# Performance work log

Measured on AMD Instinct MI355X. Metric: run time of the kernel, lower is better.

The kernel has to match this reference:

```python
import jax, jax.numpy as jnp
import numpy as np

B, S, D_IN, D_OUT = 4, 2048, 1024, 1024


def setup_inputs() -> dict:
    key = jax.random.key(0)
    ks = jax.random.split(key, 7)
    s_in = 1.0 / np.sqrt(D_IN)
    return {
        "x": jax.random.normal(ks[0], (B, S, D_IN), dtype=jnp.float32),
        "Wq": jax.random.uniform(ks[1], (D_IN, D_OUT), jnp.float32, -s_in, s_in),
        "bq": jax.random.uniform(ks[2], (D_OUT,), jnp.float32, -s_in, s_in),
        "Wk": jax.random.uniform(ks[3], (D_IN, D_OUT), jnp.float32, -s_in, s_in),
        "bk": jax.random.uniform(ks[4], (D_OUT,), jnp.float32, -s_in, s_in),
        "Wv": jax.random.uniform(ks[5], (D_IN, D_OUT), jnp.float32, -s_in, s_in),
        "bv": jax.random.uniform(ks[6], (D_OUT,), jnp.float32, -s_in, s_in),
    }


def reference(x, Wq, bq, Wk, bk, Wv, bv):
    # q,k,v: [B, S, D_OUT]
    q = jnp.einsum("bsd,de->bse", x, Wq) + bq
    k = jnp.einsum("bsd,de->bse", x, Wk) + bk
    v = jnp.einsum("bsd,de->bse", x, Wv) + bv
    scale = 1.0 / jnp.sqrt(jnp.asarray(q.shape[-1], q.dtype))
    scores = jnp.einsum("bqe,bke->bqk", q, k) * scale  # [B, S, S]
    attn = jax.nn.softmax(scores, axis=-1)
    return jnp.einsum("bqk,bke->bqe", attn, v)
```

## Files before the change

kernel.cpp:

```cpp
#include <hip/hip_runtime.h>
#include <hip/hip_bf16.h>
#include <stdint.h>


#define Bsz 4
#define Ssz 2048
#define Dsz 1024

typedef __attribute__((ext_vector_type(8))) short short8;
typedef __attribute__((ext_vector_type(4))) float floatx4;
typedef const __attribute__((address_space(1))) void* gptr_t;
typedef __attribute__((address_space(3))) void* lptr_t;

__device__ __forceinline__ ushort f32_to_bf16(float f) {
    union { float f; uint32_t u; } c; c.f = f;
    uint32_t u = c.u;
    u += 0x7fffu + ((u >> 16) & 1u);
    return (ushort)(u >> 16);
}

__global__ __launch_bounds__(256, 2) void k_qkv(
    const ushort* __restrict__ xb, const ushort* __restrict__ Wt,
    const float* __restrict__ bq, const float* __restrict__ bk,
    const float* __restrict__ bv, ushort* __restrict__ QKV,
    ushort* __restrict__ Vt)
{
    __shared__ ushort lsA[2][128 * 32];
    __shared__ ushort lsB[2][3][128 * 32];

    const int tid  = threadIdx.x;
    const int bx   = blockIdx.x;
    const int by   = blockIdx.y;
    const int row0 = by * 128;
    const int col0 = bx * 128;

    const int lane = tid & 63;
    const int wave = tid >> 6;
    const int wr   = (wave >> 1) * 64;
    const int wc   = (wave & 1) * 64;
    const int m16  = lane & 15;
    const int quad = lane >> 4;

    floatx4 acc[3][4][4];
#pragma unroll
    for (int z = 0; z < 3; z++)
#pragma unroll
        for (int i = 0; i < 4; i++)
#pragma unroll
            for (int j = 0; j < 4; j++) acc[z][i][j] = (floatx4){0.f, 0.f, 0.f, 0.f};

    const int srow = tid >> 2;
    const int skc  = (tid & 3) ^ ((srow >> 1) & 3);
    const ushort* ga = xb + (size_t)(row0 + srow) * Dsz + skc * 8;
    const ushort* gb0 = Wt + (size_t)(col0 + srow) * Dsz + skc * 8;

    const int aoff = (quad ^ ((m16 >> 1) & 3)) * 8;

    __builtin_amdgcn_global_load_lds((gptr_t)(ga),                    (lptr_t)(lsA[0] + tid * 8),        16, 0, 0);
    __builtin_amdgcn_global_load_lds((gptr_t)(ga + (size_t)64 * Dsz), (lptr_t)(lsA[0] + 2048 + tid * 8), 16, 0, 0);
#pragma unroll
    for (int z = 0; z < 3; z++) {
        const ushort* gb = gb0 + (size_t)z * Dsz * Dsz;
        __builtin_amdgcn_global_load_lds((gptr_t)(gb),                    (lptr_t)(lsB[0][z] + tid * 8),        16, 0, 0);
        __builtin_amdgcn_global_load_lds((gptr_t)(gb + (size_t)64 * Dsz), (lptr_t)(lsB[0][z] + 2048 + tid * 8), 16, 0, 0);
    }

    for (int k0 = 0; k0 < Dsz; k0 += 32) {
        const int cur = (k0 >> 5) & 1;
        __syncthreads();
        if (k0 + 32 < Dsz) {
            const int nxt = cur ^ 1;
            const int kn = k0 + 32;
            __builtin_amdgcn_global_load_lds((gptr_t)(ga + kn),                    (lptr_t)(lsA[nxt] + tid * 8),        16, 0, 0);
            __builtin_amdgcn_global_load_lds((gptr_t)(ga + kn + (size_t)64 * Dsz), (lptr_t)(lsA[nxt] + 2048 + tid * 8), 16, 0, 0);
#pragma unroll
            for (int z = 0; z < 3; z++) {
                const ushort* gb = gb0 + (size_t)z * Dsz * Dsz + kn;
                __builtin_amdgcn_global_load_lds((gptr_t)(gb),                    (lptr_t)(lsB[nxt][z] + tid * 8),        16, 0, 0);
                __builtin_amdgcn_global_load_lds((gptr_t)(gb + (size_t)64 * Dsz), (lptr_t)(lsB[nxt][z] + 2048 + tid * 8), 16, 0, 0);
            }
        }

        short8 af[4];
#pragma unroll
        for (int mi = 0; mi < 4; mi++)
            af[mi] = *(const short8*)&lsA[cur][(wr + mi * 16 + m16) * 32 + aoff];
#pragma unroll
        for (int z = 0; z < 3; z++) {
            short8 bfr[4];
#pragma unroll
            for (int ni = 0; ni < 4; ni++)
                bfr[ni] = *(const short8*)&lsB[cur][z][(wc + ni * 16 + m16) * 32 + aoff];
#pragma unroll
            for (int mi = 0; mi < 4; mi++)
#pragma unroll
                for (int ni = 0; ni < 4; ni++)
                    acc[z][mi][ni] = __builtin_amdgcn_mfma_f32_16x16x32_bf16(af[mi], bfr[ni], acc[z][mi][ni], 0, 0, 0);
        }
    }

#pragma unroll
    for (int ni = 0; ni < 4; ni++) {
        const int gcol = col0 + wc + ni * 16 + m16;
        const float bqv = bq[gcol], bkv = bk[gcol], bvv = bv[gcol];
#pragma unroll
        for (int mi = 0; mi < 4; mi++) {
            const int grow0 = row0 + wr + mi * 16 + quad * 4;
            ushort4 vpack;
#pragma unroll
            for (int j = 0; j < 4; j++) {
                QKV[(size_t)(grow0 + j) * Dsz + gcol] = f32_to_bf16((acc[0][mi][ni][j] + bqv) * 0.03125f);
                QKV[(size_t)(Bsz * Ssz) * Dsz + (size_t)(grow0 + j) * Dsz + gcol] = f32_to_bf16(acc[1][mi][ni][j] + bkv);
                const ushort vv = f32_to_bf16(acc[2][mi][ni][j] + bvv);
                if (j == 0) vpack.x = vv; else if (j == 1) vpack.y = vv;
                else if (j == 2) vpack.z = vv; else vpack.w = vv;
            }
            const int batch = grow0 >> 11;
            const int s0 = grow0 & (Ssz - 1);
            *(ushort4*)&Vt[(size_t)batch * Dsz * Ssz + (size_t)gcol * Ssz + s0] = vpack;
        }
    }
}

__global__ __launch_bounds__(512, 2) void k_scores(
    const ushort* __restrict__ QKV, ushort* __restrict__ P,
    float* __restrict__ partial)
{
    __shared__ ushort lsA[2][256 * 32];
    __shared__ ushort lsB[2][256 * 32];
    __shared__ float  red[4][256];

    const int bid = blockIdx.x;
    const int bn  = bid & 7;
    const int i   = bid >> 3;
    const int bm  = i & 7;
    const int b   = i >> 3;
    const int row0 = bm * 256;
    const int col0 = bn * 256;

    const ushort* A  = QKV + (size_t)b * Ssz * Dsz;
    const ushort* Bt = QKV + (size_t)(Bsz + b) * Ssz * Dsz;
    ushort* Pb = P + (size_t)b * Ssz * Ssz;

    const int tid  = threadIdx.x;
    const int lane = tid & 63;
    const int wave = tid >> 6;
    const int wr   = (wave >> 2) * 128;
    const int wc   = (wave & 3) * 64;
    const int m16  = lane & 15;
    const int quad = lane >> 4;

    floatx4 acc[8][4];
#pragma unroll
    for (int mi = 0; mi < 8; mi++)
#pragma unroll
        for (int ni = 0; ni < 4; ni++) acc[mi][ni] = (floatx4){0.f, 0.f, 0.f, 0.f};

    const int srow = tid >> 2;
    const int skc  = (tid & 3) ^ ((srow >> 1) & 3);
    const ushort* ga = A  + (size_t)(row0 + srow) * Dsz + skc * 8;
    const ushort* gb = Bt + (size_t)(col0 + srow) * Dsz + skc * 8;
    const int aoff = (quad ^ ((m16 >> 1) & 3)) * 8;

    __builtin_amdgcn_global_load_lds((gptr_t)(ga),                      (lptr_t)(lsA[0] + tid * 8),        16, 0, 0);
    __builtin_amdgcn_global_load_lds((gptr_t)(ga + (size_t)128 * Dsz),  (lptr_t)(lsA[0] + 4096 + tid * 8), 16, 0, 0);
    __builtin_amdgcn_global_load_lds((gptr_t)(gb),                      (lptr_t)(lsB[0] + tid * 8),        16, 0, 0);
    __builtin_amdgcn_global_load_lds((gptr_t)(gb + (size_t)128 * Dsz),  (lptr_t)(lsB[0] + 4096 + tid * 8), 16, 0, 0);

    for (int k0 = 0; k0 < Dsz; k0 += 32) {
        const int cur = (k0 >> 5) & 1;
        __syncthreads();
        if (k0 + 32 < Dsz) {
            const int nxt = cur ^ 1;
            const int kn = k0 + 32;
            __builtin_amdgcn_global_load_lds((gptr_t)(ga + kn),                      (lptr_t)(lsA[nxt] + tid * 8),        16, 0, 0);
            __builtin_amdgcn_global_load_lds((gptr_t)(ga + kn + (size_t)128 * Dsz),  (lptr_t)(lsA[nxt] + 4096 + tid * 8), 16, 0, 0);
            __builtin_amdgcn_global_load_lds((gptr_t)(gb + kn),                      (lptr_t)(lsB[nxt] + tid * 8),        16, 0, 0);
            __builtin_amdgcn_global_load_lds((gptr_t)(gb + kn + (size_t)128 * Dsz),  (lptr_t)(lsB[nxt] + 4096 + tid * 8), 16, 0, 0);
        }

        short8 af[8], bfr[4];
#pragma unroll
        for (int mi = 0; mi < 8; mi++)
            af[mi] = *(const short8*)&lsA[cur][(wr + mi * 16 + m16) * 32 + aoff];
#pragma unroll
        for (int ni = 0; ni < 4; ni++)
            bfr[ni] = *(const short8*)&lsB[cur][(wc + ni * 16 + m16) * 32 + aoff];
#pragma unroll
        for (int mi = 0; mi < 8; mi++)
#pragma unroll
            for (int ni = 0; ni < 4; ni++)
                acc[mi][ni] = __builtin_amdgcn_mfma_f32_16x16x32_bf16(af[mi], bfr[ni], acc[mi][ni], 0, 0, 0);
    }

    float rs[8][4];
#pragma unroll
    for (int mi = 0; mi < 8; mi++)
#pragma unroll
        for (int j = 0; j < 4; j++) rs[mi][j] = 0.f;
#pragma unroll
    for (int ni = 0; ni < 4; ni++) {
        const int gcol = col0 + wc + ni * 16 + m16;
#pragma unroll
        for (int mi = 0; mi < 8; mi++) {
            const int grow0 = row0 + wr + mi * 16 + quad * 4;
#pragma unroll
            for (int j = 0; j < 4; j++) {
                const float e = __expf(acc[mi][ni][j]);
                Pb[(size_t)(grow0 + j) * Ssz + gcol] = f32_to_bf16(e);
                rs[mi][j] += e;
            }
        }
    }
#pragma unroll
    for (int mi = 0; mi < 8; mi++)
#pragma unroll
        for (int j = 0; j < 4; j++) {
            float v = rs[mi][j];
            v += __shfl_xor(v, 1, 64);
            v += __shfl_xor(v, 2, 64);
            v += __shfl_xor(v, 4, 64);
            v += __shfl_xor(v, 8, 64);
            if (m16 == 0) red[wave & 3][wr + mi * 16 + quad * 4 + j] = v;
        }
    __syncthreads();
    if (tid < 256) {
        const float s = red[0][tid] + red[1][tid] + red[2][tid] + red[3][tid];
        partial[(((size_t)b * 8 + bm) * 8 + bn) * 256 + tid] = s;
    }
}

__global__ __launch_bounds__(512, 1) void k_pv(
    const ushort* __restrict__ P, const ushort* __restrict__ Vt,
    const float* __restrict__ partial, float* __restrict__ out)
{
    __shared__ ushort lsA[2][128 * 32];
    __shared__ ushort lsB[2][256 * 32];
    __shared__ float  invs[128];

    const int bid = blockIdx.x;
    const int c   = bid & 7;
    const int i   = bid >> 3;
    const int bx  = i & 3;
    const int sid = c * 8 + (i >> 2);
    const int by  = sid & 15;
    const int b   = sid >> 4;
    const int row0 = by * 128;
    const int col0 = bx * 256;

    const ushort* A  = P  + (size_t)b * Ssz * Ssz;
    const ushort* Bt = Vt + (size_t)b * Dsz * Ssz;
    float* Cout = out + (size_t)b * Ssz * Dsz;
    const float* pin = partial + (size_t)b * 8 * 8 * 256;

    const int tid  = threadIdx.x;
    const int lane = tid & 63;
    const int wave = tid >> 6;
    const int wr   = (wave >> 2) * 64;
    const int wc   = (wave & 3) * 64;
    const int m16  = lane & 15;
    const int quad = lane >> 4;

    floatx4 acc[4][4];
#pragma unroll
    for (int i2 = 0; i2 < 4; i2++)
#pragma unroll
        for (int j = 0; j < 4; j++) acc[i2][j] = (floatx4){0.f, 0.f, 0.f, 0.f};

    if (tid < 128) {
        const int r = row0 + tid;
        const float* pb = pin + ((size_t)(r >> 8) * 8) * 256 + (r & 255);
        float s = 0.f;
#pragma unroll
        for (int bn = 0; bn < 8; bn++) s += pb[bn * 256];
        invs[tid] = 1.0f / s;
    }

    const int srow = tid >> 2;
    const int skc  = (tid & 3) ^ ((srow >> 1) & 3);
    const ushort* ga = A  + (size_t)(row0 + srow) * Ssz + skc * 8;
    const ushort* gb = Bt + (size_t)(col0 + srow) * Ssz + skc * 8;
    const int aoff = (quad ^ ((m16 >> 1) & 3)) * 8;

    __builtin_amdgcn_global_load_lds((gptr_t)(ga),                      (lptr_t)(lsA[0] + tid * 8),        16, 0, 0);
    __builtin_amdgcn_global_load_lds((gptr_t)(gb),                      (lptr_t)(lsB[0] + tid * 8),        16, 0, 0);
    __builtin_amdgcn_global_load_lds((gptr_t)(gb + (size_t)128 * Ssz),  (lptr_t)(lsB[0] + 4096 + tid * 8), 16, 0, 0);

    for (int k0 = 0; k0 < Ssz; k0 += 32) {
        const int cur = (k0 >> 5) & 1;
        __syncthreads();
        if (k0 + 32 < Ssz) {
            const int nxt = cur ^ 1;
            const int kn = k0 + 32;
            __builtin_amdgcn_global_load_lds((gptr_t)(ga + kn),                      (lptr_t)(lsA[nxt] + tid * 8),        16, 0, 0);
            __builtin_amdgcn_global_load_lds((gptr_t)(gb + kn),                      (lptr_t)(lsB[nxt] + tid * 8),        16, 0, 0);
            __builtin_amdgcn_global_load_lds((gptr_t)(gb + kn + (size_t)128 * Ssz),  (lptr_t)(lsB[nxt] + 4096 + tid * 8), 16, 0, 0);
        }

        short8 af[4], bfr[4];
#pragma unroll
        for (int mi = 0; mi < 4; mi++)
            af[mi] = *(const short8*)&lsA[cur][(wr + mi * 16 + m16) * 32 + aoff];
#pragma unroll
        for (int ni = 0; ni < 4; ni++)
            bfr[ni] = *(const short8*)&lsB[cur][(wc + ni * 16 + m16) * 32 + aoff];
#pragma unroll
        for (int mi = 0; mi < 4; mi++)
#pragma unroll
            for (int ni = 0; ni < 4; ni++)
                acc[mi][ni] = __builtin_amdgcn_mfma_f32_16x16x32_bf16(af[mi], bfr[ni], acc[mi][ni], 0, 0, 0);
    }

#pragma unroll
    for (int ni = 0; ni < 4; ni++) {
        const int gcol = col0 + wc + ni * 16 + m16;
#pragma unroll
        for (int mi = 0; mi < 4; mi++) {
            const int grow0 = row0 + wr + mi * 16 + quad * 4;
            const int rl0   = wr + mi * 16 + quad * 4;
#pragma unroll
            for (int j = 0; j < 4; j++)
                Cout[(size_t)(grow0 + j) * Dsz + gcol] = acc[mi][ni][j] * invs[rl0 + j];
        }
    }
}

__global__ __launch_bounds__(256) void k_prep(
    const float* __restrict__ x, ushort* __restrict__ xb,
    const float* __restrict__ Wq, const float* __restrict__ Wk,
    const float* __restrict__ Wv, ushort* __restrict__ Wt)
{
    __shared__ float tile[32][33];
    const int bid = blockIdx.x;
    const int tid = threadIdx.x;
    if (bid < 8192) {
        int i = (bid * 256 + tid) * 4;
        float4 v = *(const float4*)(x + i);
        ushort4 o;
        o.x = f32_to_bf16(v.x); o.y = f32_to_bf16(v.y);
        o.z = f32_to_bf16(v.z); o.w = f32_to_bf16(v.w);
        *(ushort4*)(xb + i) = o;
    } else {
        const int wb = bid - 8192;
        const int z  = wb >> 10;
        const int r  = wb & 1023;
        const int nb = (r & 31) * 32;
        const int kb = (r >> 5) * 32;
        const float* W = (z == 0) ? Wq : ((z == 1) ? Wk : Wv);
        ushort* out = Wt + (size_t)z * Dsz * Dsz;
        const int tx = tid & 31, ty = tid >> 5;
#pragma unroll
        for (int j = 0; j < 32; j += 8)
            tile[ty + j][tx] = W[(size_t)(kb + ty + j) * Dsz + nb + tx];
        __syncthreads();
#pragma unroll
        for (int j = 0; j < 32; j += 8)
            out[(size_t)(nb + ty + j) * Dsz + kb + tx] = f32_to_bf16(tile[tx][ty + j]);
    }
}

extern "C" void kernel_launch(void* const* d_in, const int* in_sizes, int n_in,
                              void* d_out, int out_size, void* d_ws, size_t ws_size,
                              hipStream_t stream) {
    const float* x  = (const float*)d_in[0];
    const float* Wq = (const float*)d_in[1];
    const float* bq = (const float*)d_in[2];
    const float* Wk = (const float*)d_in[3];
    const float* bk = (const float*)d_in[4];
    const float* Wv = (const float*)d_in[5];
    const float* bv = (const float*)d_in[6];
    float* out = (float*)d_out;

    char* ws = (char*)d_ws;
    ushort* xb      = (ushort*)(ws);
    ushort* Wt      = (ushort*)(ws + 16777216);
    ushort* QKV     = (ushort*)(ws + 23068672);
    ushort* Vt      = (ushort*)(ws + 73400320);
    ushort* P       = (ushort*)(ws + 90177536);
    float*  partial = (float*) (ws + 123731968);

    k_prep<<<dim3(8192 + 3072), dim3(256), 0, stream>>>(x, xb, Wq, Wk, Wv, Wt);
    k_qkv<<<dim3(Dsz / 128, Bsz * Ssz / 128), dim3(256), 0, stream>>>(xb, Wt, bq, bk, bv, QKV, Vt);
    k_scores<<<dim3(256), dim3(512), 0, stream>>>(QKV, P, partial);
    k_pv<<<dim3(256), dim3(512), 0, stream>>>(P, Vt, partial, out);
}
```

Before: 265.6 us.

## Restructure QK^T scores GEMM into fine-grained 8-phase pipelined schedule with K=64 tiles

```diff
diff --git a/kernel.cpp b/kernel.cpp
--- a/kernel.cpp
+++ b/kernel.cpp
@@ -17,6 +17,16 @@
     uint32_t u = c.u;
     u += 0x7fffu + ((u >> 16) & 1u);
     return (ushort)(u >> 16);
+}
+
+__device__ __forceinline__ void glds16(const ushort* g, ushort* l) {
+    __builtin_amdgcn_global_load_lds((gptr_t)g, (lptr_t)l, 16, 0, 0);
+}
+
+__device__ __forceinline__ void barrier_raw() {
+    asm volatile("" ::: "memory");
+    __builtin_amdgcn_s_barrier();
+    asm volatile("" ::: "memory");
 }
 
 __global__ __launch_bounds__(256, 2) void k_qkv(
@@ -122,33 +132,61 @@
     }
 }
 
+#define RD_A(QM, PAR)                                                          \
+    _Pragma("unroll") for (int mi_ = 0; mi_ < 4; mi_++) {                      \
+        const ushort* rp_ = &lsA[(PAR) * 2 + waveM][((QM) * 64 + mi_ * 16 + m16) * 64]; \
+        a0[mi_] = *(const short8*)(rp_ + csw);                                 \
+        a1[mi_] = *(const short8*)(rp_ + (csw ^ 32));                          \
+    }
+#define RD_B(QN, PAR, SET)                                                     \
+    _Pragma("unroll") for (int nj_ = 0; nj_ < 2; nj_++) {                      \
+        const ushort* rp_ = &lsB[(PAR) * 2 + bReg][(bRow0 + (QN) * 32 + nj_ * 16 + m16) * 64]; \
+        bb[SET][nj_][0] = *(const short8*)(rp_ + csw);                         \
+        bb[SET][nj_][1] = *(const short8*)(rp_ + (csw ^ 32));                  \
+    }
+#define MM(MH, NH, SET)                                                        \
+    _Pragma("unroll") for (int mi_ = 0; mi_ < 4; mi_++)                        \
+    _Pragma("unroll") for (int nj_ = 0; nj_ < 2; nj_++) {                      \
+        acc[(MH) * 4 + mi_][(NH) * 2 + nj_] = __builtin_amdgcn_mfma_f32_16x16x32_bf16( \
+            a0[mi_], bb[SET][nj_][0], acc[(MH) * 4 + mi_][(NH) * 2 + nj_], 0, 0, 0);   \
+        acc[(MH) * 4 + mi_][(NH) * 2 + nj_] = __builtin_amdgcn_mfma_f32_16x16x32_bf16( \
+            a1[mi_], bb[SET][nj_][1], acc[(MH) * 4 + mi_][(NH) * 2 + nj_], 0, 0, 0);   \
+    }
+
 __global__ __launch_bounds__(512, 2) void k_scores(
     const ushort* __restrict__ QKV, ushort* __restrict__ P,
     float* __restrict__ partial)
 {
-    __shared__ ushort lsA[2][256 * 32];
-    __shared__ ushort lsB[2][256 * 32];
-    __shared__ float  red[4][256];
+    __shared__ __align__(16) ushort lsA[4][8192];
+    __shared__ __align__(16) ushort lsB[4][8192];
+    __shared__ float red[4][256];
 
     const int bid = blockIdx.x;
     const int bn  = bid & 7;
-    const int i   = bid >> 3;
-    const int bm  = i & 7;
-    const int b   = i >> 3;
-    const int row0 = bm * 256;
-    const int col0 = bn * 256;
-
-    const ushort* A  = QKV + (size_t)b * Ssz * Dsz;
-    const ushort* Bt = QKV + (size_t)(Bsz + b) * Ssz * Dsz;
+    const int ii  = bid >> 3;
+    const int bm  = ii & 7;
+    const int b   = ii >> 3;
+    const int row0 = bm * 256, col0 = bn * 256;
+
+    const ushort* Aq = QKV + (size_t)b * Ssz * Dsz;
+    const ushort* Bk = QKV + (size_t)(Bsz + b) * Ssz * Dsz;
     ushort* Pb = P + (size_t)b * Ssz * Ssz;
 
-    const int tid  = threadIdx.x;
-    const int lane = tid & 63;
-    const int wave = tid >> 6;
-    const int wr   = (wave >> 2) * 128;
-    const int wc   = (wave & 3) * 64;
-    const int m16  = lane & 15;
-    const int quad = lane >> 4;
+    const int tid   = threadIdx.x;
+    const int lane  = tid & 63;
+    const int wave  = tid >> 6;
+    const int m16   = lane & 15;
+    const int quad  = lane >> 4;
+    const int waveM = wave >> 2;
+    const int waveN = wave & 3;
+    const int wr    = waveM * 128;
+    const int wc    = waveN * 64;
+    const int bReg  = waveN >> 1;
+    const int bRow0 = (waveN & 1) * 64;
+    const int csw   = (quad ^ (m16 & 7)) * 8;
+
+    const int sRow = tid >> 3;
+    const int sCol = ((tid & 7) ^ (sRow & 7)) * 8;
 
     floatx4 acc[8][4];
 #pragma unroll
@@ -156,41 +194,79 @@
 #pragma unroll
         for (int ni = 0; ni < 4; ni++) acc[mi][ni] = (floatx4){0.f, 0.f, 0.f, 0.f};
 
-    const int srow = tid >> 2;
-    const int skc  = (tid & 3) ^ ((srow >> 1) & 3);
-    const ushort* ga = A  + (size_t)(row0 + srow) * Dsz + skc * 8;
-    const ushort* gb = Bt + (size_t)(col0 + srow) * Dsz + skc * 8;
-    const int aoff = (quad ^ ((m16 >> 1) & 3)) * 8;
-
-    __builtin_amdgcn_global_load_lds((gptr_t)(ga),                      (lptr_t)(lsA[0] + tid * 8),        16, 0, 0);
-    __builtin_amdgcn_global_load_lds((gptr_t)(ga + (size_t)128 * Dsz),  (lptr_t)(lsA[0] + 4096 + tid * 8), 16, 0, 0);
-    __builtin_amdgcn_global_load_lds((gptr_t)(gb),                      (lptr_t)(lsB[0] + tid * 8),        16, 0, 0);
-    __builtin_amdgcn_global_load_lds((gptr_t)(gb + (size_t)128 * Dsz),  (lptr_t)(lsB[0] + 4096 + tid * 8), 16, 0, 0);
-
-    for (int k0 = 0; k0 < Dsz; k0 += 32) {
-        const int cur = (k0 >> 5) & 1;
-        __syncthreads();
-        if (k0 + 32 < Dsz) {
-            const int nxt = cur ^ 1;
-            const int kn = k0 + 32;
-            __builtin_amdgcn_global_load_lds((gptr_t)(ga + kn),                      (lptr_t)(lsA[nxt] + tid * 8),        16, 0, 0);
-            __builtin_amdgcn_global_load_lds((gptr_t)(ga + kn + (size_t)128 * Dsz),  (lptr_t)(lsA[nxt] + 4096 + tid * 8), 16, 0, 0);
-            __builtin_amdgcn_global_load_lds((gptr_t)(gb + kn),                      (lptr_t)(lsB[nxt] + tid * 8),        16, 0, 0);
-            __builtin_amdgcn_global_load_lds((gptr_t)(gb + kn + (size_t)128 * Dsz),  (lptr_t)(lsB[nxt] + 4096 + tid * 8), 16, 0, 0);
-        }
-
-        short8 af[8], bfr[4];
-#pragma unroll
-        for (int mi = 0; mi < 8; mi++)
-            af[mi] = *(const short8*)&lsA[cur][(wr + mi * 16 + m16) * 32 + aoff];
-#pragma unroll
-        for (int ni = 0; ni < 4; ni++)
-            bfr[ni] = *(const short8*)&lsB[cur][(wc + ni * 16 + m16) * 32 + aoff];
-#pragma unroll
-        for (int mi = 0; mi < 8; mi++)
-#pragma unroll
-            for (int ni = 0; ni < 4; ni++)
-                acc[mi][ni] = __builtin_amdgcn_mfma_f32_16x16x32_bf16(af[mi], bfr[ni], acc[mi][ni], 0, 0, 0);
+    auto stA = [&](int t, int half) {
+        ushort* d = &lsA[(t & 1) * 2 + half][0] + tid * 8;
+        const ushort* s = Aq + (size_t)(row0 + half * 128 + sRow) * Dsz + t * 64 + sCol;
+        glds16(s, d);
+        glds16(s + (size_t)64 * Dsz, d + 4096);
+    };
+    auto stB = [&](int t, int half) {
+        ushort* d = &lsB[(t & 1) * 2 + half][0] + tid * 8;
+        const ushort* s = Bk + (size_t)(col0 + half * 128 + sRow) * Dsz + t * 64 + sCol;
+        glds16(s, d);
+        glds16(s + (size_t)64 * Dsz, d + 4096);
+    };
+
+    short8 a0[4], a1[4], bb[2][2][2];
+
+    stB(0, 0); stB(0, 1);
+    stA(0, 0); stA(0, 1);
+    stB(1, 0); stB(1, 1);
+    asm volatile("s_waitcnt vmcnt(4)" ::: "memory");
+    barrier_raw();
+
+    for (int it = 0; it < 8; ++it) {
+        const int t0 = 2 * it, t1 = t0 + 1;
+        const bool s2 = (t0 + 2 < 16), s3 = (t1 + 2 < 16);
+
+        RD_A(0, 0); RD_B(0, 0, 0);
+        stA(t1, 0);
+        barrier_raw();
+        __builtin_amdgcn_s_setprio(1); MM(0, 0, 0); __builtin_amdgcn_s_setprio(0);
+        barrier_raw();
+
+        RD_B(1, 0, 1);
+        stA(t1, 1);
+        barrier_raw();
+        __builtin_amdgcn_s_setprio(1); MM(0, 1, 1); __builtin_amdgcn_s_setprio(0);
+        barrier_raw();
+
+        RD_A(1, 0);
+        if (s2) stB(t0 + 2, 0);
+        barrier_raw();
+        __builtin_amdgcn_s_setprio(1); MM(1, 1, 1); __builtin_amdgcn_s_setprio(0);
+        barrier_raw();
+
+        if (s2) stB(t0 + 2, 1);
+        barrier_raw();
+        __builtin_amdgcn_s_setprio(1); MM(1, 0, 0); __builtin_amdgcn_s_setprio(0);
+        if (s2) { asm volatile("s_waitcnt vmcnt(4)" ::: "memory"); }
+        else    { asm volatile("s_waitcnt vmcnt(0)" ::: "memory"); }
+        barrier_raw();
+
+        RD_A(0, 1); RD_B(0, 1, 0);
+        if (s2) stA(t0 + 2, 0);
+        barrier_raw();
+        __builtin_amdgcn_s_setprio(1); MM(0, 0, 0); __builtin_amdgcn_s_setprio(0);
+        barrier_raw();
+
+        RD_B(1, 1, 1);
+        if (s2) stA(t0 + 2, 1);
+        barrier_raw();
+        __builtin_amdgcn_s_setprio(1); MM(0, 1, 1); __builtin_amdgcn_s_setprio(0);
+        barrier_raw();
+
+        RD_A(1, 1);
+        if (s3) stB(t1 + 2, 0);
+        barrier_raw();
+        __builtin_amdgcn_s_setprio(1); MM(1, 1, 1); __builtin_amdgcn_s_setprio(0);
+        barrier_raw();
+
+        if (s3) stB(t1 + 2, 1);
+        barrier_raw();
+        __builtin_amdgcn_s_setprio(1); MM(1, 0, 0); __builtin_amdgcn_s_setprio(0);
+        if (it < 7) { asm volatile("s_waitcnt vmcnt(4)" ::: "memory"); }
+        barrier_raw();
     }
 
     float rs[8][4];
@@ -221,7 +297,7 @@
             v += __shfl_xor(v, 2, 64);
             v += __shfl_xor(v, 4, 64);
             v += __shfl_xor(v, 8, 64);
-            if (m16 == 0) red[wave & 3][wr + mi * 16 + quad * 4 + j] = v;
+            if (m16 == 0) red[waveN][wr + mi * 16 + quad * 4 + j] = v;
         }
     __syncthreads();
     if (tid < 256) {
```

Measured after the change: 268.0 us. No clear change (+0.9%).
